# Optimization experiments

Measured on AMD Instinct MI355X. Metric: run time of the kernel, lower is better.

The kernel has to match this reference:

```python
import jax, jax.numpy as jnp
import numpy as np

CAPACITY_FACTOR = 1.25


def setup_inputs() -> dict:
    key = jax.random.key(0)
    k1, k2, k3, k4, k5, k6 = jax.random.split(key, 6)
    N, d, E, h = 8192, 1024, 8, 2816
    x = jax.random.normal(k1, (N, d), dtype=jnp.float32)
    topK_indices = jax.random.randint(k2, (N,), 0, E, dtype=jnp.int64)
    topK_scores = jax.random.uniform(k3, (N,), dtype=jnp.float32)
    Wg = jax.random.normal(k4, (E, d, h), dtype=jnp.float32) * 0.02
    Wu = jax.random.normal(k5, (E, d, h), dtype=jnp.float32) * 0.02
    Wd = jax.random.normal(k6, (E, h, d), dtype=jnp.float32) * 0.02
    return {"x": x, "topK_indices": topK_indices, "topK_scores": topK_scores,
            "Wg": Wg, "Wu": Wu, "Wd": Wd}


def reference(x, topK_indices, topK_scores, Wg, Wu, Wd):
    # x: [N, d] tokens; topK_indices: [N] top-1 expert ids; per-expert SwiGLU FFN.
    N, d = x.shape
    E = Wg.shape[0]
    capacity = int(CAPACITY_FACTOR * N / E)  # = 1280

    idx = topK_indices.astype(jnp.int32)
    onehot = jax.nn.one_hot(idx, E, dtype=jnp.int32)            # [N, E]
    # position of each token within its expert's queue (first-come-first-served)
    pos = jnp.sum((jnp.cumsum(onehot, axis=0) - 1) * onehot, axis=1)  # [N]
    kept = pos < capacity                                        # dropped tokens pass through

    # flat dispatch slot: expert*capacity + pos for kept tokens, overflow bucket otherwise
    slots = jnp.where(kept, idx * capacity + pos, E * capacity)  # [N]
    buf = jnp.zeros((E * capacity + 1, d), dtype=x.dtype).at[slots].set(x)
    xe = buf[: E * capacity].reshape(E, capacity, d)             # [E, C, d]

    # per-expert SwiGLU FFN (grouped GEMMs)
    hgate = jnp.einsum('ecd,edh->ech', xe, Wg)
    hup = jnp.einsum('ecd,edh->ech', xe, Wu)
    hact = jax.nn.silu(hgate) * hup
    out = jnp.einsum('ech,ehd->ecd', hact, Wd).reshape(E * capacity, d)
    out = jnp.concatenate([out, jnp.zeros((1, d), out.dtype)], axis=0)

    y_tok = out[slots]                                           # gather back per token
    # multiply_gate_scores=True: scale expert output by routing score; dropped -> identity
    y = jnp.where(kept[:, None], y_tok * topK_scores[:, None], x)
    return y
```

## Files before the change

kernel.cpp:

```cpp
#include <hip/hip_runtime.h>
#include <cstdint>
#include <cstddef>

#define N_TOK 8192
#define DIM   1024
#define NEXP  8
#define HID   2816
#define CAP   1280

typedef __bf16 bf16x8 __attribute__((ext_vector_type(8)));
typedef float  floatx4 __attribute__((ext_vector_type(4)));
typedef unsigned short u16x8 __attribute__((ext_vector_type(8)));

__device__ __forceinline__ unsigned short f2bf(float f) {
  return __builtin_bit_cast(unsigned short, (__bf16)f);
}

__device__ __forceinline__ void async16(void* lds, const void* g) {
  __builtin_amdgcn_global_load_lds(
      (const __attribute__((address_space(1))) void*)g,
      (__attribute__((address_space(3))) void*)lds, 16, 0, 0);
}

__global__ void route_kernel(const int* __restrict__ idx, int idx_stride,
                             int* __restrict__ slot,
                             int* __restrict__ slot_token,
                             int* __restrict__ counts) {
  __shared__ int hist[256][NEXP];
  const int t = threadIdx.x;
  int loc[NEXP];
#pragma unroll
  for (int e = 0; e < NEXP; e++) loc[e] = 0;
  const int base = t * 32;
  for (int i = 0; i < 32; i++) {
    int e = idx[(base + i) * idx_stride];
    loc[e]++;
  }
#pragma unroll
  for (int e = 0; e < NEXP; e++) hist[t][e] = loc[e];
  __syncthreads();
  if (t < NEXP) {
    int run = 0;
    for (int i = 0; i < 256; i++) { int v = hist[i][t]; hist[i][t] = run; run += v; }
    counts[t] = run < CAP ? run : CAP;
  }
  __syncthreads();
  int b2[NEXP];
#pragma unroll
  for (int e = 0; e < NEXP; e++) b2[e] = hist[t][e];
  for (int i = 0; i < 32; i++) {
    const int n = base + i;
    const int e = idx[n * idx_stride];
    const int p = b2[e]++;
    if (p < CAP) {
      const int s = e * CAP + p;
      slot[n] = s;
      slot_token[s] = n;
    } else {
      slot[n] = -1;
    }
  }
}

__global__ void dispatch_kernel(const float* __restrict__ x,
                                const int* __restrict__ slot,
                                unsigned short* __restrict__ xe,
                                float* __restrict__ y) {
  const int n = blockIdx.x;
  const int t = threadIdx.x;
  const int s = slot[n];
  const float4 v = ((const float4*)(x + (size_t)n * DIM))[t];
  if (s >= 0) {
    ushort4 b;
    b.x = f2bf(v.x); b.y = f2bf(v.y); b.z = f2bf(v.z); b.w = f2bf(v.w);
    ((ushort4*)(xe + (size_t)s * DIM))[t] = b;
  } else {
    ((float4*)(y + (size_t)n * DIM))[t] = v;
  }
}

__global__ __launch_bounds__(256)
void transpose_cvt(const float* __restrict__ in,
                   unsigned short* __restrict__ out,
                   const int R, const int C) {
  __shared__ float tile[64][65];
  const int e = blockIdx.z;
  const float* ib = in + (size_t)e * R * C;
  unsigned short* ob = out + (size_t)e * R * C;
  const int t = threadIdx.x;
  const int c0 = blockIdx.x * 64, r0 = blockIdx.y * 64;
  const int lr = t >> 4;
  const int lc = (t & 15) * 4;
#pragma unroll
  for (int i = 0; i < 4; i++) {
    const float4 v = *(const float4*)(ib + (size_t)(r0 + lr + i * 16) * C + c0 + lc);
    tile[lr + i * 16][lc + 0] = v.x;
    tile[lr + i * 16][lc + 1] = v.y;
    tile[lr + i * 16][lc + 2] = v.z;
    tile[lr + i * 16][lc + 3] = v.w;
  }
  __syncthreads();
  const int oc = t >> 2;
  const int sub = t & 3;
#pragma unroll
  for (int half = 0; half < 2; half++) {
    const int rch = sub + half * 4;
    u16x8 o;
#pragma unroll
    for (int j = 0; j < 8; j++) o[j] = f2bf(tile[rch * 8 + j][oc]);
    *(u16x8*)(ob + (size_t)(c0 + oc) * R + r0 + rch * 8) = o;
  }
}

__global__ __launch_bounds__(256)
void gateup_gemm(const unsigned short* __restrict__ A,
                 const unsigned short* __restrict__ Bg,
                 const unsigned short* __restrict__ Bu,
                 const int* __restrict__ counts,
                 unsigned short* __restrict__ hact) {
  const int bid = blockIdx.x;
  const int xcd = bid & 7;
  const int slot = bid >> 3;
  const int m = slot % 10;
  const int cgl = slot / 10;
  const int cg = xcd + 8 * cgl;
  const int n = cg % 44;
  const int e = cg / 44;

  const int cnt = counts[e];
  const int m0 = m * 128;
  if (m0 >= cnt) return;
  const int n0 = n * 64;

  __shared__ char smem[16384];

  const int t = threadIdx.x;
  const int lane = t & 63;
  const int w = t >> 6;
  const int wr = w >> 1;
  const int wc = w & 1;

  const int sr = t >> 2;
  const int sc = (t & 3) ^ ((sr >> 1) & 3);
  const unsigned short* aP  = A  + (size_t)e * CAP * DIM + (size_t)(m0 + sr) * DIM + sc * 8;
  const unsigned short* aP1 = aP + (size_t)64 * DIM;
  const unsigned short* bgP = Bg + (size_t)e * HID * DIM + (size_t)(n0 + sr) * DIM + sc * 8;
  const unsigned short* buP = Bu + (size_t)e * HID * DIM + (size_t)(n0 + sr) * DIM + sc * 8;
  char* lA0 = smem + t * 16;
  char* lA1 = smem + 4096 + t * 16;
  char* lBg = smem + 8192 + t * 16;
  char* lBu = smem + 12288 + t * 16;

  floatx4 accg[4][2] = {};
  floatx4 accu[4][2] = {};

  const int mrow = wr * 64 + (lane & 15);
  const int ncol = wc * 32 + (lane & 15);
  const int q = lane >> 4;
  const int kqA = ((q ^ ((mrow >> 1) & 3)) * 16);
  const int kqB = ((q ^ ((ncol >> 1) & 3)) * 16);

  for (int kk = 0; kk < DIM; kk += 32) {
    async16(lA0, aP); async16(lA1, aP1);
    async16(lBg, bgP); async16(lBu, buP);
    aP += 32; aP1 += 32; bgP += 32; buP += 32;
    __syncthreads();
    bf16x8 af[4], gf[2], uf[2];
#pragma unroll
    for (int i = 0; i < 4; i++)
      af[i] = *(const bf16x8*)(smem + (mrow + i * 16) * 64 + kqA);
#pragma unroll
    for (int i = 0; i < 2; i++) {
      gf[i] = *(const bf16x8*)(smem + 8192 + (ncol + i * 16) * 64 + kqB);
      uf[i] = *(const bf16x8*)(smem + 12288 + (ncol + i * 16) * 64 + kqB);
    }
#pragma unroll
    for (int mi = 0; mi < 4; mi++)
#pragma unroll
      for (int ni = 0; ni < 2; ni++) {
        accg[mi][ni] = __builtin_amdgcn_mfma_f32_16x16x32_bf16(
            af[mi], gf[ni], accg[mi][ni], 0, 0, 0);
        accu[mi][ni] = __builtin_amdgcn_mfma_f32_16x16x32_bf16(
            af[mi], uf[ni], accu[mi][ni], 0, 0, 0);
      }
    __syncthreads();
  }

  const int quad = lane >> 4;
  const int cl = lane & 15;
  unsigned short* ob = hact + (size_t)e * CAP * HID;
#pragma unroll
  for (int mi = 0; mi < 4; mi++)
#pragma unroll
    for (int r = 0; r < 4; r++) {
      const int row = m0 + wr * 64 + mi * 16 + quad * 4 + r;
      const size_t rb = (size_t)row * HID;
#pragma unroll
      for (int ni = 0; ni < 2; ni++) {
        const int col = n0 + wc * 32 + ni * 16 + cl;
        const float g = accg[mi][ni][r];
        const float u = accu[mi][ni][r];
        ob[rb + col] = f2bf(g / (1.0f + __expf(-g)) * u);
      }
    }
}

__global__ __launch_bounds__(256)
void down_gemm(const unsigned short* __restrict__ A,
               const unsigned short* __restrict__ Bt,
               const int* __restrict__ counts,
               const int* __restrict__ slot_token,
               const float* __restrict__ scores,
               float* __restrict__ y) {
  const int bid = blockIdx.x;
  const int xcd = bid & 7;
  const int slot = bid >> 3;
  const int m = slot % 10;
  const int cgl = slot / 10;
  const int cg = xcd + 8 * cgl;
  const int n = cg % 8;
  const int e = cg / 8;

  const int cnt = counts[e];
  const int m0 = m * 128;
  if (m0 >= cnt) return;
  const int n0 = n * 128;

  __shared__ char smem[16384];

  const int t = threadIdx.x;
  const int lane = t & 63;
  const int w = t >> 6;
  const int wr = w >> 1;
  const int wc = w & 1;

  const int sr = t >> 2;
  const int sc = (t & 3) ^ ((sr >> 1) & 3);
  const unsigned short* aP  = A + (size_t)e * CAP * HID + (size_t)(m0 + sr) * HID + sc * 8;
  const unsigned short* aP1 = aP + (size_t)64 * HID;
  const unsigned short* bP  = Bt + (size_t)e * DIM * HID + (size_t)(n0 + sr) * HID + sc * 8;
  const unsigned short* bP1 = bP + (size_t)64 * HID;
  char* lA0 = smem + t * 16;
  char* lA1 = smem + 4096 + t * 16;
  char* lB0 = smem + 8192 + t * 16;
  char* lB1 = smem + 12288 + t * 16;

  floatx4 acc[4][4] = {};

  const int mrow = wr * 64 + (lane & 15);
  const int ncol = wc * 64 + (lane & 15);
  const int q = lane >> 4;
  const int kqA = ((q ^ ((mrow >> 1) & 3)) * 16);
  const int kqB = ((q ^ ((ncol >> 1) & 3)) * 16);

  for (int kk = 0; kk < HID; kk += 32) {
    async16(lA0, aP); async16(lA1, aP1);
    async16(lB0, bP); async16(lB1, bP1);
    aP += 32; aP1 += 32; bP += 32; bP1 += 32;
    __syncthreads();
    bf16x8 af[4], bfr[4];
#pragma unroll
    for (int i = 0; i < 4; i++)
      af[i] = *(const bf16x8*)(smem + (mrow + i * 16) * 64 + kqA);
#pragma unroll
    for (int i = 0; i < 4; i++)
      bfr[i] = *(const bf16x8*)(smem + 8192 + (ncol + i * 16) * 64 + kqB);
#pragma unroll
    for (int mi = 0; mi < 4; mi++)
#pragma unroll
      for (int ni = 0; ni < 4; ni++)
        acc[mi][ni] = __builtin_amdgcn_mfma_f32_16x16x32_bf16(
            af[mi], bfr[ni], acc[mi][ni], 0, 0, 0);
    __syncthreads();
  }

  const int quad = lane >> 4;
  const int cl = lane & 15;
#pragma unroll
  for (int mi = 0; mi < 4; mi++)
#pragma unroll
    for (int r = 0; r < 4; r++) {
      const int row = m0 + wr * 64 + mi * 16 + quad * 4 + r;
      if (row < cnt) {
        const int tok = slot_token[e * CAP + row];
        const float s = scores[tok];
        float* yr = y + (size_t)tok * DIM;
#pragma unroll
        for (int ni = 0; ni < 4; ni++) {
          const int col = n0 + wc * 64 + ni * 16 + cl;
          yr[col] = acc[mi][ni][r] * s;
        }
      }
    }
}

extern "C" void kernel_launch(void* const* d_in, const int* in_sizes, int n_in,
                              void* d_out, int out_size, void* d_ws, size_t ws_size,
                              hipStream_t stream) {
  const float* x      = (const float*)d_in[0];
  const int*   idx    = (const int*)d_in[1];
  const float* scores = (const float*)d_in[2];
  const float* Wg     = (const float*)d_in[3];
  const float* Wu     = (const float*)d_in[4];
  const float* Wd     = (const float*)d_in[5];
  float* y = (float*)d_out;

  const int idx_stride = (in_sizes[1] == 2 * N_TOK) ? 2 : 1;

  char* ws = (char*)d_ws;
  size_t off = 0;
  auto alloc = [&](size_t b) -> char* {
    char* p = ws + off;
    off += (b + 255) & ~(size_t)255;
    return p;
  };
  int* counts            = (int*)alloc(NEXP * 4);
  int* slot              = (int*)alloc((size_t)N_TOK * 4);
  int* slot_token        = (int*)alloc((size_t)NEXP * CAP * 4);
  unsigned short* xe     = (unsigned short*)alloc((size_t)NEXP * CAP * DIM * 2);
  unsigned short* hact   = (unsigned short*)alloc((size_t)NEXP * CAP * HID * 2);
  unsigned short* wg_t   = (unsigned short*)alloc((size_t)NEXP * DIM * HID * 2);
  unsigned short* wu_t   = (unsigned short*)alloc((size_t)NEXP * DIM * HID * 2);
  unsigned short* wd_t   = (unsigned short*)alloc((size_t)NEXP * DIM * HID * 2);
  (void)ws_size; (void)n_in; (void)out_size;

  route_kernel<<<1, 256, 0, stream>>>(idx, idx_stride, slot, slot_token, counts);
  dispatch_kernel<<<N_TOK, 256, 0, stream>>>(x, slot, xe, y);

  transpose_cvt<<<dim3(HID / 64, DIM / 64, NEXP), 256, 0, stream>>>(Wg, wg_t, DIM, HID);
  transpose_cvt<<<dim3(HID / 64, DIM / 64, NEXP), 256, 0, stream>>>(Wu, wu_t, DIM, HID);
  transpose_cvt<<<dim3(DIM / 64, HID / 64, NEXP), 256, 0, stream>>>(Wd, wd_t, HID, DIM);

  gateup_gemm<<<8 * 44 * 10, 256, 0, stream>>>(xe, wg_t, wu_t, counts, hact);
  down_gemm<<<8 * 8 * 10, 256, 0, stream>>>(hact, wd_t, counts, slot_token, scores, y);
}
```

Measured before the change: 560.9 us.

## Double K-step in GEMMs, merge weight transposes, parallelize routing scan

```diff
diff --git a/kernel.cpp b/kernel.cpp
--- a/kernel.cpp
+++ b/kernel.cpp
@@ -22,43 +22,84 @@
       (__attribute__((address_space(3))) void*)lds, 16, 0, 0);
 }
 
-__global__ void route_kernel(const int* __restrict__ idx, int idx_stride,
-                             int* __restrict__ slot,
-                             int* __restrict__ slot_token,
-                             int* __restrict__ counts) {
-  __shared__ int hist[256][NEXP];
+__global__ __launch_bounds__(256)
+void route_kernel(const int* __restrict__ idx, int idx_stride,
+                  int* __restrict__ slot,
+                  int* __restrict__ slot_token,
+                  int* __restrict__ counts) {
+  __shared__ int hist[256][9];
   const int t = threadIdx.x;
-  int loc[NEXP];
-#pragma unroll
-  for (int e = 0; e < NEXP; e++) loc[e] = 0;
-  const int base = t * 32;
+
+  int myidx[32];
+  if (idx_stride == 1) {
+    const int4* p = (const int4*)(idx + (size_t)t * 32);
+#pragma unroll
+    for (int i = 0; i < 8; i++) {
+      const int4 v = p[i];
+      myidx[4 * i + 0] = v.x; myidx[4 * i + 1] = v.y;
+      myidx[4 * i + 2] = v.z; myidx[4 * i + 3] = v.w;
+    }
+  } else {
+    const int4* p = (const int4*)(idx + (size_t)t * 64);
+#pragma unroll
+    for (int i = 0; i < 16; i++) {
+      const int4 v = p[i];
+      myidx[2 * i + 0] = v.x; myidx[2 * i + 1] = v.z;
+    }
+  }
+
+  int c[NEXP];
+#pragma unroll
+  for (int k = 0; k < NEXP; k++) c[k] = 0;
+#pragma unroll
   for (int i = 0; i < 32; i++) {
-    int e = idx[(base + i) * idx_stride];
-    loc[e]++;
-  }
-#pragma unroll
-  for (int e = 0; e < NEXP; e++) hist[t][e] = loc[e];
+    const int e = myidx[i];
+#pragma unroll
+    for (int k = 0; k < NEXP; k++) c[k] += (e == k);
+  }
+#pragma unroll
+  for (int k = 0; k < NEXP; k++) hist[t][k] = c[k];
   __syncthreads();
-  if (t < NEXP) {
-    int run = 0;
-    for (int i = 0; i < 256; i++) { int v = hist[i][t]; hist[i][t] = run; run += v; }
-    counts[t] = run < CAP ? run : CAP;
+
+  const int lane = t & 63;
+  const int w = t >> 6;
+#pragma unroll
+  for (int which = 0; which < 2; which++) {
+    const int e = w * 2 + which;
+    int v[4], s = 0;
+#pragma unroll
+    for (int i = 0; i < 4; i++) { v[i] = hist[lane * 4 + i][e]; s += v[i]; }
+    int x = s;
+#pragma unroll
+    for (int d = 1; d < 64; d <<= 1) {
+      const int n = __shfl_up(x, d, 64);
+      if (lane >= d) x += n;
+    }
+    int run = x - s;
+#pragma unroll
+    for (int i = 0; i < 4; i++) { const int tmp = v[i]; hist[lane * 4 + i][e] = run; run += tmp; }
+    if (lane == 63) counts[e] = run < CAP ? run : CAP;
   }
   __syncthreads();
-  int b2[NEXP];
-#pragma unroll
-  for (int e = 0; e < NEXP; e++) b2[e] = hist[t][e];
+
+  int b[NEXP];
+#pragma unroll
+  for (int k = 0; k < NEXP; k++) b[k] = hist[t][k];
   for (int i = 0; i < 32; i++) {
-    const int n = base + i;
-    const int e = idx[n * idx_stride];
-    const int p = b2[e]++;
+    const int e = myidx[i];
+    int p = 0;
+#pragma unroll
+    for (int k = 0; k < NEXP; k++) p += (e == k) ? b[k] : 0;
+    const int n = t * 32 + i;
     if (p < CAP) {
-      const int s = e * CAP + p;
-      slot[n] = s;
-      slot_token[s] = n;
+      const int s2 = e * CAP + p;
+      slot[n] = s2;
+      slot_token[s2] = n;
     } else {
       slot[n] = -1;
     }
+#pragma unroll
+    for (int k = 0; k < NEXP; k++) b[k] += (e == k);
   }
 }
 
@@ -80,15 +121,25 @@
 }
 
 __global__ __launch_bounds__(256)
-void transpose_cvt(const float* __restrict__ in,
-                   unsigned short* __restrict__ out,
-                   const int R, const int C) {
+void transpose_cvt_all(const float* __restrict__ Wg, const float* __restrict__ Wu,
+                       const float* __restrict__ Wd,
+                       unsigned short* __restrict__ wg_t,
+                       unsigned short* __restrict__ wu_t,
+                       unsigned short* __restrict__ wd_t) {
   __shared__ float tile[64][65];
-  const int e = blockIdx.z;
+  const int mat = blockIdx.y, e = blockIdx.z, tid = blockIdx.x;
+  const float* in;
+  unsigned short* outp;
+  int R, C;
+  if (mat == 0)      { in = Wg; outp = wg_t; R = DIM; C = HID; }
+  else if (mat == 1) { in = Wu; outp = wu_t; R = DIM; C = HID; }
+  else               { in = Wd; outp = wd_t; R = HID; C = DIM; }
+  const int tilesC = C / 64;
+  const int r0 = (tid / tilesC) * 64, c0 = (tid % tilesC) * 64;
   const float* ib = in + (size_t)e * R * C;
-  unsigned short* ob = out + (size_t)e * R * C;
+  unsigned short* ob = outp + (size_t)e * R * C;
   const int t = threadIdx.x;
-  const int c0 = blockIdx.x * 64, r0 = blockIdx.y * 64;
+
   const int lr = t >> 4;
   const int lc = (t & 15) * 4;
 #pragma unroll
@@ -100,15 +151,14 @@
     tile[lr + i * 16][lc + 3] = v.w;
   }
   __syncthreads();
-  const int oc = t >> 2;
-  const int sub = t & 3;
-#pragma unroll
-  for (int half = 0; half < 2; half++) {
-    const int rch = sub + half * 4;
+  const int chunk = t & 7;
+#pragma unroll
+  for (int h = 0; h < 2; h++) {
+    const int row = (t >> 3) + 32 * h;
     u16x8 o;
 #pragma unroll
-    for (int j = 0; j < 8; j++) o[j] = f2bf(tile[rch * 8 + j][oc]);
-    *(u16x8*)(ob + (size_t)(c0 + oc) * R + r0 + rch * 8) = o;
+    for (int j = 0; j < 8; j++) o[j] = f2bf(tile[chunk * 8 + j][row]);
+    *(u16x8*)(ob + (size_t)(c0 + row) * R + r0 + chunk * 8) = o;
   }
 }
 
@@ -120,9 +170,9 @@
                  unsigned short* __restrict__ hact) {
   const int bid = blockIdx.x;
   const int xcd = bid & 7;
-  const int slot = bid >> 3;
-  const int m = slot % 10;
-  const int cgl = slot / 10;
+  const int slotb = bid >> 3;
+  const int m = slotb % 10;
+  const int cgl = slotb / 10;
   const int cg = xcd + 8 * cgl;
   const int n = cg % 44;
   const int e = cg / 44;
@@ -132,7 +182,10 @@
   if (m0 >= cnt) return;
   const int n0 = n * 64;
 
-  __shared__ char smem[16384];
+  __shared__ char smem[32768];
+  char* const lA  = smem;
+  char* const lBg = smem + 16384;
+  char* const lBu = smem + 24576;
 
   const int t = threadIdx.x;
   const int lane = t & 63;
@@ -140,54 +193,68 @@
   const int wr = w >> 1;
   const int wc = w & 1;
 
-  const int sr = t >> 2;
-  const int sc = (t & 3) ^ ((sr >> 1) & 3);
-  const unsigned short* aP  = A  + (size_t)e * CAP * DIM + (size_t)(m0 + sr) * DIM + sc * 8;
-  const unsigned short* aP1 = aP + (size_t)64 * DIM;
-  const unsigned short* bgP = Bg + (size_t)e * HID * DIM + (size_t)(n0 + sr) * DIM + sc * 8;
-  const unsigned short* buP = Bu + (size_t)e * HID * DIM + (size_t)(n0 + sr) * DIM + sc * 8;
-  char* lA0 = smem + t * 16;
-  char* lA1 = smem + 4096 + t * 16;
-  char* lBg = smem + 8192 + t * 16;
-  char* lBu = smem + 12288 + t * 16;
+  const int srow = t >> 3;
+  const int schk = (t & 7) ^ (srow & 7);
+  const unsigned short* aP[4];
+  const unsigned short* bgP[2];
+  const unsigned short* buP[2];
+#pragma unroll
+  for (int r = 0; r < 4; r++)
+    aP[r] = A + (size_t)e * CAP * DIM + (size_t)(m0 + r * 32 + srow) * DIM + schk * 8;
+#pragma unroll
+  for (int r = 0; r < 2; r++) {
+    bgP[r] = Bg + (size_t)e * HID * DIM + (size_t)(n0 + r * 32 + srow) * DIM + schk * 8;
+    buP[r] = Bu + (size_t)e * HID * DIM + (size_t)(n0 + r * 32 + srow) * DIM + schk * 8;
+  }
 
   floatx4 accg[4][2] = {};
   floatx4 accu[4][2] = {};
 
-  const int mrow = wr * 64 + (lane & 15);
-  const int ncol = wc * 32 + (lane & 15);
-  const int q = lane >> 4;
-  const int kqA = ((q ^ ((mrow >> 1) & 3)) * 16);
-  const int kqB = ((q ^ ((ncol >> 1) & 3)) * 16);
-
-  for (int kk = 0; kk < DIM; kk += 32) {
-    async16(lA0, aP); async16(lA1, aP1);
-    async16(lBg, bgP); async16(lBu, buP);
-    aP += 32; aP1 += 32; bgP += 32; buP += 32;
+  const int cl = lane & 15;
+  const int quad = lane >> 4;
+  const int x0 = quad ^ (lane & 7);
+  const int x1 = x0 ^ 4;
+  const int mrB = (wr * 64 + cl) * 128;
+  const int ncB = (wc * 32 + cl) * 128;
+
+  for (int kk = 0; kk < DIM; kk += 64) {
+#pragma unroll
+    for (int r = 0; r < 4; r++) async16(lA + r * 4096 + t * 16, aP[r]);
+#pragma unroll
+    for (int r = 0; r < 2; r++) {
+      async16(lBg + r * 4096 + t * 16, bgP[r]);
+      async16(lBu + r * 4096 + t * 16, buP[r]);
+    }
+#pragma unroll
+    for (int r = 0; r < 4; r++) aP[r] += 64;
+#pragma unroll
+    for (int r = 0; r < 2; r++) { bgP[r] += 64; buP[r] += 64; }
     __syncthreads();
-    bf16x8 af[4], gf[2], uf[2];
-#pragma unroll
-    for (int i = 0; i < 4; i++)
-      af[i] = *(const bf16x8*)(smem + (mrow + i * 16) * 64 + kqA);
-#pragma unroll
-    for (int i = 0; i < 2; i++) {
-      gf[i] = *(const bf16x8*)(smem + 8192 + (ncol + i * 16) * 64 + kqB);
-      uf[i] = *(const bf16x8*)(smem + 12288 + (ncol + i * 16) * 64 + kqB);
-    }
-#pragma unroll
-    for (int mi = 0; mi < 4; mi++)
+#pragma unroll
+    for (int ks = 0; ks < 2; ks++) {
+      const int x = ks ? x1 : x0;
+      bf16x8 af[4], gf[2], uf[2];
+#pragma unroll
+      for (int mi = 0; mi < 4; mi++)
+        af[mi] = *(const bf16x8*)(lA + mrB + mi * 2048 + x * 16);
 #pragma unroll
       for (int ni = 0; ni < 2; ni++) {
-        accg[mi][ni] = __builtin_amdgcn_mfma_f32_16x16x32_bf16(
-            af[mi], gf[ni], accg[mi][ni], 0, 0, 0);
-        accu[mi][ni] = __builtin_amdgcn_mfma_f32_16x16x32_bf16(
-            af[mi], uf[ni], accu[mi][ni], 0, 0, 0);
+        gf[ni] = *(const bf16x8*)(lBg + ncB + ni * 2048 + x * 16);
+        uf[ni] = *(const bf16x8*)(lBu + ncB + ni * 2048 + x * 16);
       }
+#pragma unroll
+      for (int mi = 0; mi < 4; mi++)
+#pragma unroll
+        for (int ni = 0; ni < 2; ni++) {
+          accg[mi][ni] = __builtin_amdgcn_mfma_f32_16x16x32_bf16(
+              af[mi], gf[ni], accg[mi][ni], 0, 0, 0);
+          accu[mi][ni] = __builtin_amdgcn_mfma_f32_16x16x32_bf16(
+              af[mi], uf[ni], accu[mi][ni], 0, 0, 0);
+        }
+    }
     __syncthreads();
   }
 
-  const int quad = lane >> 4;
-  const int cl = lane & 15;
   unsigned short* ob = hact + (size_t)e * CAP * HID;
 #pragma unroll
   for (int mi = 0; mi < 4; mi++)
@@ -214,9 +281,9 @@
                float* __restrict__ y) {
   const int bid = blockIdx.x;
   const int xcd = bid & 7;
-  const int slot = bid >> 3;
-  const int m = slot % 10;
-  const int cgl = slot / 10;
+  const int slotb = bid >> 3;
+  const int m = slotb % 10;
+  const int cgl = slotb / 10;
   const int cg = xcd + 8 * cgl;
   const int n = cg % 8;
   const int e = cg / 8;
@@ -226,7 +293,9 @@
   if (m0 >= cnt) return;
   const int n0 = n * 128;
 
-  __shared__ char smem[16384];
+  __shared__ char smem[32768];
+  char* const lA = smem;
+  char* const lB = smem + 16384;
 
   const int t = threadIdx.x;
   const int lane = t & 63;
@@ -234,48 +303,54 @@
   const int wr = w >> 1;
   const int wc = w & 1;
 
-  const int sr = t >> 2;
-  const int sc = (t & 3) ^ ((sr >> 1) & 3);
-  const unsigned short* aP  = A + (size_t)e * CAP * HID + (size_t)(m0 + sr) * HID + sc * 8;
-  const unsigned short* aP1 = aP + (size_t)64 * HID;
-  const unsigned short* bP  = Bt + (size_t)e * DIM * HID + (size_t)(n0 + sr) * HID + sc * 8;
-  const unsigned short* bP1 = bP + (size_t)64 * HID;
-  char* lA0 = smem + t * 16;
-  char* lA1 = smem + 4096 + t * 16;
-  char* lB0 = smem + 8192 + t * 16;
-  char* lB1 = smem + 12288 + t * 16;
+  const int srow = t >> 3;
+  const int schk = (t & 7) ^ (srow & 7);
+  const unsigned short* aP[4];
+  const unsigned short* bP[4];
+#pragma unroll
+  for (int r = 0; r < 4; r++) {
+    aP[r] = A  + (size_t)e * CAP * HID + (size_t)(m0 + r * 32 + srow) * HID + schk * 8;
+    bP[r] = Bt + (size_t)e * DIM * HID + (size_t)(n0 + r * 32 + srow) * HID + schk * 8;
+  }
 
   floatx4 acc[4][4] = {};
 
-  const int mrow = wr * 64 + (lane & 15);
-  const int ncol = wc * 64 + (lane & 15);
-  const int q = lane >> 4;
-  const int kqA = ((q ^ ((mrow >> 1) & 3)) * 16);
-  const int kqB = ((q ^ ((ncol >> 1) & 3)) * 16);
-
-  for (int kk = 0; kk < HID; kk += 32) {
-    async16(lA0, aP); async16(lA1, aP1);
-    async16(lB0, bP); async16(lB1, bP1);
-    aP += 32; aP1 += 32; bP += 32; bP1 += 32;
+  const int cl = lane & 15;
+  const int quad = lane >> 4;
+  const int x0 = quad ^ (lane & 7);
+  const int x1 = x0 ^ 4;
+  const int mrB = (wr * 64 + cl) * 128;
+  const int ncB = (wc * 64 + cl) * 128;
+
+  for (int kk = 0; kk < HID; kk += 64) {
+#pragma unroll
+    for (int r = 0; r < 4; r++) {
+      async16(lA + r * 4096 + t * 16, aP[r]);
+      async16(lB + r * 4096 + t * 16, bP[r]);
+      aP[r] += 64; bP[r] += 64;
+    }
     __syncthreads();
-    bf16x8 af[4], bfr[4];
-#pragma unroll
-    for (int i = 0; i < 4; i++)
-      af[i] = *(const bf16x8*)(smem + (mrow + i * 16) * 64 + kqA);
-#pragma unroll
-    for (int i = 0; i < 4; i++)
-      bfr[i] = *(const bf16x8*)(smem + 8192 + (ncol + i * 16) * 64 + kqB);
-#pragma unroll
-    for (int mi = 0; mi < 4; mi++)
+#pragma unroll
+    for (int ks = 0; ks < 2; ks++) {
+      const int x = ks ? x1 : x0;
+      bf16x8 af[4], bfr[4];
+#pragma unroll
+      for (int mi = 0; mi < 4; mi++)
+        af[mi] = *(const bf16x8*)(lA + mrB + mi * 2048 + x * 16);
 #pragma unroll
       for (int ni = 0; ni < 4; ni++)
-        acc[mi][ni] = __builtin_amdgcn_mfma_f32_16x16x32_bf16(
-            af[mi], bfr[ni], acc[mi][ni], 0, 0, 0);
+        bfr[ni] = *(const bf16x8*)(lB + ncB + ni * 2048 + x * 16);
+#pragma unroll
+      for (int mi = 0; mi < 4; mi++)
+#pragma unroll
+        for (int ni = 0; ni < 4; ni++)
+          acc[mi][ni] = __builtin_amdgcn_mfma_f32_16x16x32_bf16(
+              af[mi], bfr[ni], acc[mi][ni], 0, 0, 0);
+    }
     __syncthreads();
   }
 
-  const int quad = lane >> 4;
-  const int cl = lane & 15;
+  const int clc = lane & 15;
 #pragma unroll
   for (int mi = 0; mi < 4; mi++)
 #pragma unroll
@@ -287,7 +362,7 @@
         float* yr = y + (size_t)tok * DIM;
 #pragma unroll
         for (int ni = 0; ni < 4; ni++) {
-          const int col = n0 + wc * 64 + ni * 16 + cl;
+          const int col = n0 + wc * 64 + ni * 16 + clc;
           yr[col] = acc[mi][ni][r] * s;
         }
       }
@@ -327,9 +402,7 @@
   route_kernel<<<1, 256, 0, stream>>>(idx, idx_stride, slot, slot_token, counts);
   dispatch_kernel<<<N_TOK, 256, 0, stream>>>(x, slot, xe, y);
 
-  transpose_cvt<<<dim3(HID / 64, DIM / 64, NEXP), 256, 0, stream>>>(Wg, wg_t, DIM, HID);
-  transpose_cvt<<<dim3(HID / 64, DIM / 64, NEXP), 256, 0, stream>>>(Wu, wu_t, DIM, HID);
-  transpose_cvt<<<dim3(DIM / 64, HID / 64, NEXP), 256, 0, stream>>>(Wd, wd_t, HID, DIM);
+  transpose_cvt_all<<<dim3(704, 3, NEXP), 256, 0, stream>>>(Wg, Wu, Wd, wg_t, wu_t, wd_t);
 
   gateup_gemm<<<8 * 44 * 10, 256, 0, stream>>>(xe, wg_t, wu_t, counts, hact);
   down_gemm<<<8 * 8 * 10, 256, 0, stream>>>(hact, wd_t, counts, slot_token, scores, y);
```

Result: slower. 585.3 us (+4.3%).
